# Kernel tuning notes

Hardware: AMD Instinct MI355X
Metric: run time of the kernel (lower is better)

## Reference

```python
import jax, jax.numpy as jnp
import numpy as np

N, IN_C, OUT_C = 8192, 256, 256


def setup_inputs() -> dict:
    key = jax.random.key(0)
    k1, k2, k3 = jax.random.split(key, 3)
    x = jax.random.normal(k1, (N, IN_C), dtype=jnp.float32)
    adj = jax.random.uniform(k2, (N, N), dtype=jnp.float32)
    # learned parameter: torch.rand(in_channels, out_channels)
    w = jax.random.uniform(k3, (IN_C, OUT_C), dtype=jnp.float32)
    return {"x": x, "adj": adj, "w": w}


def reference(x, adj, w):
    # A = adj + I
    A = adj + jnp.eye(adj.shape[0], dtype=adj.dtype)
    # D_hat = sqrt(inv(diag(rowsum(A)))) == diag(deg^{-1/2}) since D is diagonal
    deg = jnp.sum(A, axis=1)                      # [N]
    d_isqrt = jax.lax.rsqrt(deg)                  # [N]
    # A_hat = D_hat @ A @ D_hat  ==  row/col scaling by d^{-1/2}
    A_hat = A * d_isqrt[:, None] * d_isqrt[None, :]
    # ELU((A_hat @ x) @ w)
    h = jnp.matmul(A_hat, x)                      # [N, in_c]
    return jax.nn.elu(jnp.matmul(h, w))           # [N, out_c]
```

## Files before the change

### kernel.cpp

```cpp
#include <hip/hip_runtime.h>
#include <stdint.h>

#define N_NODES 8192
#define CH 256
#define MT 32
#define BK 64
#define KB_COUNT (N_NODES / BK)
#define ZROWS 16

typedef __bf16 bf16x8 __attribute__((ext_vector_type(8)));
typedef float f32x4 __attribute__((ext_vector_type(4)));
typedef unsigned int u32x4 __attribute__((ext_vector_type(4)));

__device__ __forceinline__ void async_copy16(const void* g, void* l) {
  __builtin_amdgcn_global_load_lds(
      (const __attribute__((address_space(1))) void*)(uintptr_t)g,
      (__attribute__((address_space(3))) void*)(uint32_t)(uintptr_t)l,
      16, 0, 0);
}

__device__ __forceinline__ unsigned short f32_to_bf16_rne(float f) {
  unsigned u = __float_as_uint(f);
  u += 0x7FFFu + ((u >> 16) & 1u);
  return (unsigned short)(u >> 16);
}

__global__ void __launch_bounds__(256) k_deg(const float* __restrict__ adj,
                                             float* __restrict__ dsq) {
  const int wave = threadIdx.x >> 6, lane = threadIdx.x & 63;
  const int row = blockIdx.x * 4 + wave;
  const f32x4* ar = (const f32x4*)(adj + (size_t)row * N_NODES);
  float s0 = 0.f, s1 = 0.f, s2 = 0.f, s3 = 0.f;
#pragma unroll
  for (int i = 0; i < 8; ++i) {
    f32x4 a = ar[lane + 64 * (4 * i + 0)];
    f32x4 b = ar[lane + 64 * (4 * i + 1)];
    f32x4 c = ar[lane + 64 * (4 * i + 2)];
    f32x4 d = ar[lane + 64 * (4 * i + 3)];
    s0 += (a.x + a.y) + (a.z + a.w);
    s1 += (b.x + b.y) + (b.z + b.w);
    s2 += (c.x + c.y) + (c.z + c.w);
    s3 += (d.x + d.y) + (d.z + d.w);
  }
  float s = (s0 + s1) + (s2 + s3);
#pragma unroll
  for (int off = 32; off > 0; off >>= 1) s += __shfl_down(s, off, 64);
  if (lane == 0) dsq[row] = rsqrtf(s + 1.0f);
}

__global__ void __launch_bounds__(256) k_zy(const float* __restrict__ x,
                                            const float* __restrict__ w,
                                            const float* __restrict__ dsq,
                                            float* __restrict__ z,
                                            unsigned short* __restrict__ yt) {
  __shared__ float xs[ZROWS][CH];
  const int r0 = blockIdx.x * ZROWS;
  const int t = threadIdx.x;
#pragma unroll
  for (int r = 0; r < ZROWS; ++r) xs[r][t] = x[(size_t)(r0 + r) * CH + t];
  __syncthreads();
  float acc[ZROWS];
#pragma unroll
  for (int r = 0; r < ZROWS; ++r) acc[r] = 0.f;
  for (int k = 0; k < CH; k += 8) {
    float wv[8];
#pragma unroll
    for (int u = 0; u < 8; ++u) wv[u] = w[(size_t)(k + u) * CH + t];
#pragma unroll
    for (int r = 0; r < ZROWS; ++r) {
#pragma unroll
      for (int u = 0; u < 8; ++u) acc[r] += xs[r][k + u] * wv[u];
    }
  }
#pragma unroll
  for (int r = 0; r < ZROWS; ++r) z[(size_t)(r0 + r) * CH + t] = acc[r];
#pragma unroll
  for (int r = 0; r < ZROWS; ++r)
    yt[(size_t)t * N_NODES + r0 + r] = f32_to_bf16_rne(dsq[r0 + r] * acc[r]);
}

__global__ void __launch_bounds__(256, 1) k_gemm1(const float* __restrict__ adj,
                                                  const unsigned short* __restrict__ yt,
                                                  const float* __restrict__ z,
                                                  const float* __restrict__ dsq,
                                                  float* __restrict__ out) {
  __shared__ __align__(16) float As[2][MT * BK];
  __shared__ __align__(16) unsigned short Bs[2][CH * BK];

  const int tid = threadIdx.x;
  const int wave = tid >> 6;
  const int lane = tid & 63;
  const int m0 = blockIdx.x * MT;
  const int lr = lane & 15;
  const int lq = lane >> 4;

  const float* ag[2];
  int aoffu[2];
#pragma unroll
  for (int q = 0; q < 2; ++q) {
    int i = wave * 2 + q;
    int s = 64 * i + lane;
    int row = s >> 4;
    int c16 = (lane & 15) ^ (row & 15);
    ag[q] = adj + (size_t)(m0 + row) * N_NODES + c16 * 4;
    aoffu[q] = 64 * i * 16;
  }
  const unsigned short* bg[8];
  int boffu[8];
#pragma unroll
  for (int q = 0; q < 8; ++q) {
    int i = wave * 8 + q;
    int s = 64 * i + lane;
    int n = s >> 3;
    int c8 = (lane & 7) ^ (n & 7);
    bg[q] = yt + (size_t)n * N_NODES + c8 * 8;
    boffu[q] = 64 * i * 16;
  }

  f32x4 acc[2][4];
#pragma unroll
  for (int i = 0; i < 2; ++i)
#pragma unroll
    for (int j = 0; j < 4; ++j) acc[i][j] = (f32x4){0.f, 0.f, 0.f, 0.f};

  auto issue = [&](int b, int k0) {
    char* aL = (char*)&As[b][0];
    char* bL = (char*)&Bs[b][0];
#pragma unroll
    for (int q = 0; q < 2; ++q) async_copy16(ag[q] + k0, aL + aoffu[q]);
#pragma unroll
    for (int q = 0; q < 8; ++q) async_copy16(bg[q] + k0, bL + boffu[q]);
  };

  issue(0, 0);

  for (int kb = 0; kb < KB_COUNT; ++kb) {
    const int b = kb & 1;
    __syncthreads();
    if (kb + 1 < KB_COUNT) issue(b ^ 1, (kb + 1) * BK);

    const char* aB = (const char*)&As[b][0];
    const char* bB = (const char*)&Bs[b][0];

#pragma unroll
    for (int k32 = 0; k32 < 2; ++k32) {
      bf16x8 afr[2];
#pragma unroll
      for (int mt = 0; mt < 2; ++mt) {
        int row = mt * 16 + lr;
        int c16 = k32 * 8 + lq * 2;
        int s0 = row * 16 + ((c16) ^ (row & 15));
        int s1 = row * 16 + ((c16 + 1) ^ (row & 15));
        f32x4 r0 = *(const f32x4*)(aB + s0 * 16);
        f32x4 r1 = *(const f32x4*)(aB + s1 * 16);
        u32x4 pk;
        pk.x = __builtin_amdgcn_perm(__float_as_uint(r0.y), __float_as_uint(r0.x), 0x07060302u);
        pk.y = __builtin_amdgcn_perm(__float_as_uint(r0.w), __float_as_uint(r0.z), 0x07060302u);
        pk.z = __builtin_amdgcn_perm(__float_as_uint(r1.y), __float_as_uint(r1.x), 0x07060302u);
        pk.w = __builtin_amdgcn_perm(__float_as_uint(r1.w), __float_as_uint(r1.z), 0x07060302u);
        afr[mt] = __builtin_bit_cast(bf16x8, pk);
      }
#pragma unroll
      for (int nt = 0; nt < 4; ++nt) {
        int n = wave * 64 + nt * 16 + lr;
        int c8 = k32 * 4 + lq;
        int s = n * 8 + (c8 ^ (n & 7));
        bf16x8 bfr = *(const bf16x8*)(bB + s * 16);
        acc[0][nt] = __builtin_amdgcn_mfma_f32_16x16x32_bf16(afr[0], bfr, acc[0][nt], 0, 0, 0);
        acc[1][nt] = __builtin_amdgcn_mfma_f32_16x16x32_bf16(afr[1], bfr, acc[1][nt], 0, 0, 0);
      }
    }
  }

#pragma unroll
  for (int mt = 0; mt < 2; ++mt) {
#pragma unroll
    for (int r = 0; r < 4; ++r) {
      int row = m0 + mt * 16 + lq * 4 + r;
      float di = dsq[row];
#pragma unroll
      for (int nt = 0; nt < 4; ++nt) {
        int col = wave * 64 + nt * 16 + lr;
        float v = acc[mt][nt][r];
        v = di * (v + di * z[(size_t)row * CH + col]);
        v = v > 0.f ? v : expm1f(v);
        out[(size_t)row * CH + col] = v;
      }
    }
  }
}

extern "C" void kernel_launch(void* const* d_in, const int* in_sizes, int n_in,
                              void* d_out, int out_size, void* d_ws, size_t ws_size,
                              hipStream_t stream) {
  const float* x = (const float*)d_in[0];
  const float* adj = (const float*)d_in[1];
  const float* w = (const float*)d_in[2];
  float* out = (float*)d_out;

  float* dsq = (float*)d_ws;
  unsigned short* yt = (unsigned short*)((char*)d_ws + 32768);
  float* z = (float*)((char*)d_ws + 32768 + (size_t)CH * N_NODES * 2);

  k_deg<<<N_NODES / 4, 256, 0, stream>>>(adj, dsq);
  k_zy<<<N_NODES / ZROWS, 256, 0, stream>>>(x, w, dsq, z, yt);
  k_gemm1<<<N_NODES / MT, 256, 0, stream>>>(adj, yt, z, dsq, out);
}
```

Baseline: 524.5 us.

## Pre-convert adjacency to bf16 during degree pass and widen GEMM to 8 waves

The degree-reduction pass now also writes a bf16 copy of adj, and the GEMM streams that copy instead of fp32. This halves the GEMM's A-operand bandwidth and removes the in-loop fp32-to-bf16 repacking, at the cost of an extra 128MB write. The z computation is merged into the degree kernel, the y transpose becomes a separate kernel with vectorized stores, and the GEMM runs 512 threads with a narrower per-wave N tile.

```diff
diff --git a/kernel.cpp b/kernel.cpp
--- a/kernel.cpp
+++ b/kernel.cpp
@@ -5,12 +5,14 @@
 #define CH 256
 #define MT 32
 #define BK 64
-#define KB_COUNT (N_NODES / BK)
+#define KB_COUNT 128
 #define ZROWS 16
+#define ZBLOCKS (N_NODES / ZROWS)
+#define DEGBLOCKS (N_NODES / 4)
 
 typedef __bf16 bf16x8 __attribute__((ext_vector_type(8)));
 typedef float f32x4 __attribute__((ext_vector_type(4)));
-typedef unsigned int u32x4 __attribute__((ext_vector_type(4)));
+typedef unsigned short u16x4 __attribute__((ext_vector_type(4)));
 
 __device__ __forceinline__ void async_copy16(const void* g, void* l) {
   __builtin_amdgcn_global_load_lds(
@@ -25,66 +27,92 @@
   return (unsigned short)(u >> 16);
 }
 
-__global__ void __launch_bounds__(256) k_deg(const float* __restrict__ adj,
-                                             float* __restrict__ dsq) {
-  const int wave = threadIdx.x >> 6, lane = threadIdx.x & 63;
-  const int row = blockIdx.x * 4 + wave;
-  const f32x4* ar = (const f32x4*)(adj + (size_t)row * N_NODES);
-  float s0 = 0.f, s1 = 0.f, s2 = 0.f, s3 = 0.f;
-#pragma unroll
-  for (int i = 0; i < 8; ++i) {
-    f32x4 a = ar[lane + 64 * (4 * i + 0)];
-    f32x4 b = ar[lane + 64 * (4 * i + 1)];
-    f32x4 c = ar[lane + 64 * (4 * i + 2)];
-    f32x4 d = ar[lane + 64 * (4 * i + 3)];
-    s0 += (a.x + a.y) + (a.z + a.w);
-    s1 += (b.x + b.y) + (b.z + b.w);
-    s2 += (c.x + c.y) + (c.z + c.w);
-    s3 += (d.x + d.y) + (d.z + d.w);
-  }
-  float s = (s0 + s1) + (s2 + s3);
-#pragma unroll
-  for (int off = 32; off > 0; off >>= 1) s += __shfl_down(s, off, 64);
-  if (lane == 0) dsq[row] = rsqrtf(s + 1.0f);
-}
-
-__global__ void __launch_bounds__(256) k_zy(const float* __restrict__ x,
-                                            const float* __restrict__ w,
-                                            const float* __restrict__ dsq,
-                                            float* __restrict__ z,
-                                            unsigned short* __restrict__ yt) {
+__device__ __forceinline__ u16x4 f32x4_to_bf16_rne(f32x4 v) {
+  u16x4 r;
+  r.x = f32_to_bf16_rne(v.x);
+  r.y = f32_to_bf16_rne(v.y);
+  r.z = f32_to_bf16_rne(v.z);
+  r.w = f32_to_bf16_rne(v.w);
+  return r;
+}
+
+__global__ void __launch_bounds__(256) k_pass1(const float* __restrict__ x,
+                                               const float* __restrict__ w,
+                                               const float* __restrict__ adj,
+                                               float* __restrict__ z,
+                                               float* __restrict__ dsq,
+                                               unsigned short* __restrict__ adjb) {
   __shared__ float xs[ZROWS][CH];
-  const int r0 = blockIdx.x * ZROWS;
+  if (blockIdx.x < ZBLOCKS) {
+    const int r0 = blockIdx.x * ZROWS;
+    const int t = threadIdx.x;
+#pragma unroll
+    for (int r = 0; r < ZROWS; ++r) xs[r][t] = x[(size_t)(r0 + r) * CH + t];
+    __syncthreads();
+    float acc[ZROWS];
+#pragma unroll
+    for (int r = 0; r < ZROWS; ++r) acc[r] = 0.f;
+    for (int k = 0; k < CH; k += 8) {
+      float wv[8];
+#pragma unroll
+      for (int u = 0; u < 8; ++u) wv[u] = w[(size_t)(k + u) * CH + t];
+#pragma unroll
+      for (int r = 0; r < ZROWS; ++r) {
+#pragma unroll
+        for (int u = 0; u < 8; ++u) acc[r] += xs[r][k + u] * wv[u];
+      }
+    }
+#pragma unroll
+    for (int r = 0; r < ZROWS; ++r) z[(size_t)(r0 + r) * CH + t] = acc[r];
+  } else {
+    const int wave = threadIdx.x >> 6, lane = threadIdx.x & 63;
+    const int row = (blockIdx.x - ZBLOCKS) * 4 + wave;
+    const f32x4* ar = (const f32x4*)(adj + (size_t)row * N_NODES);
+    u16x4* br = (u16x4*)(adjb + (size_t)row * N_NODES);
+    float s0 = 0.f, s1 = 0.f, s2 = 0.f, s3 = 0.f;
+#pragma unroll
+    for (int i = 0; i < 8; ++i) {
+      f32x4 a = ar[lane + 64 * (4 * i + 0)];
+      f32x4 b = ar[lane + 64 * (4 * i + 1)];
+      f32x4 c = ar[lane + 64 * (4 * i + 2)];
+      f32x4 d = ar[lane + 64 * (4 * i + 3)];
+      br[lane + 64 * (4 * i + 0)] = f32x4_to_bf16_rne(a);
+      br[lane + 64 * (4 * i + 1)] = f32x4_to_bf16_rne(b);
+      br[lane + 64 * (4 * i + 2)] = f32x4_to_bf16_rne(c);
+      br[lane + 64 * (4 * i + 3)] = f32x4_to_bf16_rne(d);
+      s0 += (a.x + a.y) + (a.z + a.w);
+      s1 += (b.x + b.y) + (b.z + b.w);
+      s2 += (c.x + c.y) + (c.z + c.w);
+      s3 += (d.x + d.y) + (d.z + d.w);
+    }
+    float s = (s0 + s1) + (s2 + s3);
+#pragma unroll
+    for (int off = 32; off > 0; off >>= 1) s += __shfl_down(s, off, 64);
+    if (lane == 0) dsq[row] = rsqrtf(s + 1.0f);
+  }
+}
+
+__global__ void __launch_bounds__(256) k_y(const float* __restrict__ z,
+                                           const float* __restrict__ dsq,
+                                           unsigned short* __restrict__ yt) {
+  const int r0 = blockIdx.x * 16;
   const int t = threadIdx.x;
-#pragma unroll
-  for (int r = 0; r < ZROWS; ++r) xs[r][t] = x[(size_t)(r0 + r) * CH + t];
-  __syncthreads();
-  float acc[ZROWS];
-#pragma unroll
-  for (int r = 0; r < ZROWS; ++r) acc[r] = 0.f;
-  for (int k = 0; k < CH; k += 8) {
-    float wv[8];
-#pragma unroll
-    for (int u = 0; u < 8; ++u) wv[u] = w[(size_t)(k + u) * CH + t];
-#pragma unroll
-    for (int r = 0; r < ZROWS; ++r) {
-#pragma unroll
-      for (int u = 0; u < 8; ++u) acc[r] += xs[r][k + u] * wv[u];
-    }
-  }
-#pragma unroll
-  for (int r = 0; r < ZROWS; ++r) z[(size_t)(r0 + r) * CH + t] = acc[r];
-#pragma unroll
-  for (int r = 0; r < ZROWS; ++r)
-    yt[(size_t)t * N_NODES + r0 + r] = f32_to_bf16_rne(dsq[r0 + r] * acc[r]);
-}
-
-__global__ void __launch_bounds__(256, 1) k_gemm1(const float* __restrict__ adj,
+  unsigned short vals[16];
+#pragma unroll
+  for (int r = 0; r < 16; ++r)
+    vals[r] = f32_to_bf16_rne(dsq[r0 + r] * z[(size_t)(r0 + r) * CH + t]);
+  *(u16x4*)&yt[(size_t)t * N_NODES + r0 + 0] = *(u16x4*)&vals[0];
+  *(u16x4*)&yt[(size_t)t * N_NODES + r0 + 4] = *(u16x4*)&vals[4];
+  *(u16x4*)&yt[(size_t)t * N_NODES + r0 + 8] = *(u16x4*)&vals[8];
+  *(u16x4*)&yt[(size_t)t * N_NODES + r0 + 12] = *(u16x4*)&vals[12];
+}
+
+__global__ void __launch_bounds__(512, 1) k_gemm1(const unsigned short* __restrict__ adjb,
                                                   const unsigned short* __restrict__ yt,
                                                   const float* __restrict__ z,
                                                   const float* __restrict__ dsq,
                                                   float* __restrict__ out) {
-  __shared__ __align__(16) float As[2][MT * BK];
+  __shared__ __align__(16) unsigned short As[2][MT * BK];
   __shared__ __align__(16) unsigned short Bs[2][CH * BK];
 
   const int tid = threadIdx.x;
@@ -94,42 +122,41 @@
   const int lr = lane & 15;
   const int lq = lane >> 4;
 
-  const float* ag[2];
-  int aoffu[2];
-#pragma unroll
-  for (int q = 0; q < 2; ++q) {
-    int i = wave * 2 + q;
-    int s = 64 * i + lane;
-    int row = s >> 4;
-    int c16 = (lane & 15) ^ (row & 15);
-    ag[q] = adj + (size_t)(m0 + row) * N_NODES + c16 * 4;
-    aoffu[q] = 64 * i * 16;
-  }
-  const unsigned short* bg[8];
-  int boffu[8];
-#pragma unroll
-  for (int q = 0; q < 8; ++q) {
-    int i = wave * 8 + q;
-    int s = 64 * i + lane;
-    int n = s >> 3;
+  const bool hasA = wave < 4;
+  const unsigned short* ag;
+  int aoffu;
+  {
+    int i = hasA ? wave : 0;
+    int p = 64 * i + lane;
+    int r = p >> 3;
+    int c8 = (lane & 7) ^ (r & 7);
+    ag = adjb + (size_t)(m0 + r) * N_NODES + c8 * 8;
+    aoffu = 1024 * i;
+  }
+  const unsigned short* bg[4];
+  int boffu[4];
+#pragma unroll
+  for (int q = 0; q < 4; ++q) {
+    int i = wave * 4 + q;
+    int p = 64 * i + lane;
+    int n = p >> 3;
     int c8 = (lane & 7) ^ (n & 7);
     bg[q] = yt + (size_t)n * N_NODES + c8 * 8;
-    boffu[q] = 64 * i * 16;
-  }
-
-  f32x4 acc[2][4];
+    boffu[q] = 1024 * i;
+  }
+
+  f32x4 acc[2][2];
 #pragma unroll
   for (int i = 0; i < 2; ++i)
 #pragma unroll
-    for (int j = 0; j < 4; ++j) acc[i][j] = (f32x4){0.f, 0.f, 0.f, 0.f};
+    for (int j = 0; j < 2; ++j) acc[i][j] = (f32x4){0.f, 0.f, 0.f, 0.f};
 
   auto issue = [&](int b, int k0) {
     char* aL = (char*)&As[b][0];
     char* bL = (char*)&Bs[b][0];
-#pragma unroll
-    for (int q = 0; q < 2; ++q) async_copy16(ag[q] + k0, aL + aoffu[q]);
-#pragma unroll
-    for (int q = 0; q < 8; ++q) async_copy16(bg[q] + k0, bL + boffu[q]);
+    if (hasA) async_copy16(ag + k0, aL + aoffu);
+#pragma unroll
+    for (int q = 0; q < 4; ++q) async_copy16(bg[q] + k0, bL + boffu[q]);
   };
 
   issue(0, 0);
@@ -148,24 +175,16 @@
 #pragma unroll
       for (int mt = 0; mt < 2; ++mt) {
         int row = mt * 16 + lr;
-        int c16 = k32 * 8 + lq * 2;
-        int s0 = row * 16 + ((c16) ^ (row & 15));
-        int s1 = row * 16 + ((c16 + 1) ^ (row & 15));
-        f32x4 r0 = *(const f32x4*)(aB + s0 * 16);
-        f32x4 r1 = *(const f32x4*)(aB + s1 * 16);
-        u32x4 pk;
-        pk.x = __builtin_amdgcn_perm(__float_as_uint(r0.y), __float_as_uint(r0.x), 0x07060302u);
-        pk.y = __builtin_amdgcn_perm(__float_as_uint(r0.w), __float_as_uint(r0.z), 0x07060302u);
-        pk.z = __builtin_amdgcn_perm(__float_as_uint(r1.y), __float_as_uint(r1.x), 0x07060302u);
-        pk.w = __builtin_amdgcn_perm(__float_as_uint(r1.w), __float_as_uint(r1.z), 0x07060302u);
-        afr[mt] = __builtin_bit_cast(bf16x8, pk);
-      }
-#pragma unroll
-      for (int nt = 0; nt < 4; ++nt) {
-        int n = wave * 64 + nt * 16 + lr;
         int c8 = k32 * 4 + lq;
-        int s = n * 8 + (c8 ^ (n & 7));
-        bf16x8 bfr = *(const bf16x8*)(bB + s * 16);
+        int p = row * 8 + (c8 ^ (row & 7));
+        afr[mt] = *(const bf16x8*)(aB + p * 16);
+      }
+#pragma unroll
+      for (int nt = 0; nt < 2; ++nt) {
+        int n = wave * 32 + nt * 16 + lr;
+        int c8 = k32 * 4 + lq;
+        int p = n * 8 + (c8 ^ (n & 7));
+        bf16x8 bfr = *(const bf16x8*)(bB + p * 16);
         acc[0][nt] = __builtin_amdgcn_mfma_f32_16x16x32_bf16(afr[0], bfr, acc[0][nt], 0, 0, 0);
         acc[1][nt] = __builtin_amdgcn_mfma_f32_16x16x32_bf16(afr[1], bfr, acc[1][nt], 0, 0, 0);
       }
@@ -179,8 +198,8 @@
       int row = m0 + mt * 16 + lq * 4 + r;
       float di = dsq[row];
 #pragma unroll
-      for (int nt = 0; nt < 4; ++nt) {
-        int col = wave * 64 + nt * 16 + lr;
+      for (int nt = 0; nt < 2; ++nt) {
+        int col = wave * 32 + nt * 16 + lr;
         float v = acc[mt][nt][r];
         v = di * (v + di * z[(size_t)row * CH + col]);
         v = v > 0.f ? v : expm1f(v);
@@ -200,9 +219,10 @@
 
   float* dsq = (float*)d_ws;
   unsigned short* yt = (unsigned short*)((char*)d_ws + 32768);
-  float* z = (float*)((char*)d_ws + 32768 + (size_t)CH * N_NODES * 2);
-
-  k_deg<<<N_NODES / 4, 256, 0, stream>>>(adj, dsq);
-  k_zy<<<N_NODES / ZROWS, 256, 0, stream>>>(x, w, dsq, z, yt);
-  k_gemm1<<<N_NODES / MT, 256, 0, stream>>>(adj, yt, z, dsq, out);
-}
+  float* z = (float*)((char*)d_ws + 4227072);
+  unsigned short* adjb = (unsigned short*)((char*)d_ws + 12615680);
+
+  k_pass1<<<ZBLOCKS + DEGBLOCKS, 256, 0, stream>>>(x, w, adj, z, dsq, adjb);
+  k_y<<<N_NODES / 16, 256, 0, stream>>>(z, dsq, yt);
+  k_gemm1<<<N_NODES / MT, 512, 0, stream>>>(adjb, yt, z, dsq, out);
+}
```

Result: faster. 506.1 us (-3.5%).
